# Kernel optimization log

Hardware: AMD Instinct MI355X
Metric: run time of the kernel (lower is better)

## Reference

```python
import jax, jax.numpy as jnp
import numpy as np

EMBED_DIM = 512
NUM_HEADS = 8
HEAD_DIM = EMBED_DIM // NUM_HEADS
SCALING = HEAD_DIM ** (-0.5)
LAMBDA = 1.0
T = 128
B = 8


def setup_inputs() -> dict:
    key = jax.random.key(0)
    ks = jax.random.split(key, 8)
    d = EMBED_DIM
    # xavier-uniform-ish scale for weights
    w_lim = float(np.sqrt(6.0 / (3 * d + d)))
    o_lim = float(np.sqrt(6.0 / (d + d)))
    return {
        "query": jax.random.normal(ks[0], (T, B, d), jnp.float32),
        "key": jax.random.normal(ks[1], (T, B, d), jnp.float32),
        "value": jax.random.normal(ks[2], (T, B, d), jnp.float32),
        "correlation_bias": jax.random.normal(ks[3], (B, T, T, T), jnp.float32) * 0.1,
        "in_proj_weight": jax.random.uniform(ks[4], (3 * d, d), jnp.float32, -w_lim, w_lim),
        "in_proj_bias": jnp.zeros((3 * d,), jnp.float32),
        "out_w": jax.random.uniform(ks[5], (d, d), jnp.float32, -o_lim, o_lim),
        "out_b": jnp.zeros((d,), jnp.float32),
    }


def reference(query, key, value, correlation_bias, in_proj_weight, in_proj_bias, out_w, out_b):
    tgt_len, bsz, d = query.shape
    h, hd = NUM_HEADS, HEAD_DIM
    # split packed in-projection
    q = query @ in_proj_weight[:d].T + in_proj_bias[:d]
    k = key @ in_proj_weight[d:2 * d].T + in_proj_bias[d:2 * d]
    v = value @ in_proj_weight[2 * d:].T + in_proj_bias[2 * d:]
    q = q * SCALING
    # [T, B, D] -> [B*H, T, hd]
    q = q.reshape(tgt_len, bsz * h, hd).transpose(1, 0, 2)
    k = k.reshape(tgt_len, bsz * h, hd).transpose(1, 0, 2)
    v = v.reshape(tgt_len, bsz * h, hd).transpose(1, 0, 2)
    # trilinear score cube: [B*H, Tq, Tk, Tv]
    scores = jnp.einsum('iat,ibt,ict->iabc', q, k, v)
    # expand correlation bias over heads: [B,Tq,Tk,Tv] -> [B*H,Tq,Tk,Tv]
    bias = jnp.broadcast_to(
        correlation_bias[:, None], (bsz, h, tgt_len, tgt_len, tgt_len)
    ).reshape(bsz * h, tgt_len, tgt_len, tgt_len)
    scores = scores + LAMBDA * bias
    # mean/max fusion over Tv, softmax over Tk
    fused = jnp.mean(scores, axis=-1) + jnp.max(scores, axis=-1)
    w = jax.nn.softmax(fused.astype(jnp.float32), axis=-1).astype(fused.dtype)
    # bmm with q (note: attends over q itself, Tk == Tq required)
    attn = jnp.einsum('iab,ibd->iad', w, q)
    attn = attn.transpose(1, 0, 2).reshape(tgt_len, bsz, d)
    return attn @ out_w.T + out_b
```

## Files before the change

### kernel.cpp

```cpp
#include <hip/hip_runtime.h>
#include <math.h>

#define SCALING 0.125f

typedef __attribute__((ext_vector_type(8))) short short8;
typedef __attribute__((ext_vector_type(4))) float f32x4;

static __device__ __forceinline__ unsigned short bf16r(float x) {
  unsigned int u = __float_as_uint(x);
  u += 0x7fffu + ((u >> 16) & 1u);
  return (unsigned short)(u >> 16);
}
static __device__ __forceinline__ float bf16f(unsigned short h) {
  return __uint_as_float(((unsigned int)h) << 16);
}
static __device__ __forceinline__ unsigned int pk_bf16(float lo, float hi) {
  unsigned int ua = __float_as_uint(lo);
  unsigned int ub = __float_as_uint(hi);
  ua += 0x7fffu + ((ua >> 16) & 1u);
  ub += 0x7fffu + ((ub >> 16) & 1u);
  return __builtin_amdgcn_perm(ub, ua, 0x07060302u);
}
static __device__ __forceinline__ void split4(float4 x, ushort4& h, ushort4& l) {
  h.x = bf16r(x.x); l.x = bf16r(x.x - bf16f(h.x));
  h.y = bf16r(x.y); l.y = bf16r(x.y - bf16f(h.y));
  h.z = bf16r(x.z); l.z = bf16r(x.z - bf16f(h.z));
  h.w = bf16r(x.w); l.w = bf16r(x.w - bf16f(h.w));
}
union U4S8 { uint4 u; short8 s; };

__global__ __launch_bounds__(256)
void prep_kernel(const float* __restrict__ query,
                 const float* __restrict__ key,
                 const float* __restrict__ value,
                 const float* __restrict__ W,
                 const float* __restrict__ out_w,
                 unsigned short* __restrict__ Xh,
                 unsigned short* __restrict__ Xl,
                 unsigned short* __restrict__ Wh,
                 unsigned short* __restrict__ Wl,
                 unsigned short* __restrict__ Owh,
                 unsigned short* __restrict__ Owl) {
  const int t = blockIdx.x * 256 + threadIdx.x;
  const int e = t * 4;
  const float* __restrict__ src;
  unsigned short *dh, *dl;
  if (e < 1572864) {
    const int g = e >> 19, j = e & 524287;
    src = (g == 0 ? query : g == 1 ? key : value) + j;
    dh = Xh + e; dl = Xl + e;
  } else if (e < 2359296) {
    const int j = e - 1572864;
    src = W + j; dh = Wh + j; dl = Wl + j;
  } else {
    const int j = e - 2359296;
    src = out_w + j; dh = Owh + j; dl = Owl + j;
  }
  const float4 v = *(const float4*)src;
  ushort4 hh, ll;
  split4(v, hh, ll);
  *(ushort4*)dh = hh;
  *(ushort4*)dl = ll;
}

__global__ __launch_bounds__(256)
void projmm_kernel(const unsigned short* __restrict__ Xh,
                   const unsigned short* __restrict__ Xl,
                   const unsigned short* __restrict__ Wh,
                   const unsigned short* __restrict__ Wl,
                   const float* __restrict__ bias,
                   float* __restrict__ qh, float* __restrict__ kh,
                   unsigned short* __restrict__ vh) {
  __shared__ __align__(16) unsigned short Ah[64 * 72];
  __shared__ __align__(16) unsigned short Al[64 * 72];
  __shared__ __align__(16) unsigned short Bh[64 * 72];
  __shared__ __align__(16) unsigned short Bl[64 * 72];
  const int n0 = blockIdx.x * 64;
  const int g = n0 >> 9;
  const unsigned short* __restrict__ Xgh = Xh + g * 524288;
  const unsigned short* __restrict__ Xgl = Xl + g * 524288;
  const int m0 = blockIdx.y * 64;
  const int tid = threadIdx.x;
  const int w = tid >> 6, lane = tid & 63;
  const int quad = lane >> 4, n15 = lane & 15;
  const int srow = tid >> 2;
  const int scol = (tid & 3) * 16;

  f32x4 acc[4];
#pragma unroll
  for (int nt = 0; nt < 4; ++nt) acc[nt] = (f32x4){0.f, 0.f, 0.f, 0.f};

  uint4 rah0, rah1, ral0, ral1, rbh0, rbh1, rbl0, rbl1;
  {
    const int ar = (m0 + srow) * 512 + scol;
    const int br = (n0 + srow) * 512 + scol;
    rah0 = *(const uint4*)&Xgh[ar];     rah1 = *(const uint4*)&Xgh[ar + 8];
    ral0 = *(const uint4*)&Xgl[ar];     ral1 = *(const uint4*)&Xgl[ar + 8];
    rbh0 = *(const uint4*)&Wh[br];      rbh1 = *(const uint4*)&Wh[br + 8];
    rbl0 = *(const uint4*)&Wl[br];      rbl1 = *(const uint4*)&Wl[br + 8];
  }

  for (int k0 = 0; k0 < 512; k0 += 64) {
    __syncthreads();
    *(uint4*)&Ah[srow * 72 + scol] = rah0; *(uint4*)&Ah[srow * 72 + scol + 8] = rah1;
    *(uint4*)&Al[srow * 72 + scol] = ral0; *(uint4*)&Al[srow * 72 + scol + 8] = ral1;
    *(uint4*)&Bh[srow * 72 + scol] = rbh0; *(uint4*)&Bh[srow * 72 + scol + 8] = rbh1;
    *(uint4*)&Bl[srow * 72 + scol] = rbl0; *(uint4*)&Bl[srow * 72 + scol + 8] = rbl1;
    __syncthreads();
    if (k0 + 64 < 512) {
      const int ar = (m0 + srow) * 512 + k0 + 64 + scol;
      const int br = (n0 + srow) * 512 + k0 + 64 + scol;
      rah0 = *(const uint4*)&Xgh[ar];   rah1 = *(const uint4*)&Xgh[ar + 8];
      ral0 = *(const uint4*)&Xgl[ar];   ral1 = *(const uint4*)&Xgl[ar + 8];
      rbh0 = *(const uint4*)&Wh[br];    rbh1 = *(const uint4*)&Wh[br + 8];
      rbl0 = *(const uint4*)&Wl[br];    rbl1 = *(const uint4*)&Wl[br + 8];
    }
#pragma unroll
    for (int kk = 0; kk < 2; ++kk) {
      short8 ah = *(const short8*)&Ah[(w * 16 + n15) * 72 + kk * 32 + quad * 8];
      short8 al = *(const short8*)&Al[(w * 16 + n15) * 72 + kk * 32 + quad * 8];
#pragma unroll
      for (int nt = 0; nt < 4; ++nt) {
        short8 bh = *(const short8*)&Bh[(nt * 16 + n15) * 72 + kk * 32 + quad * 8];
        short8 bl = *(const short8*)&Bl[(nt * 16 + n15) * 72 + kk * 32 + quad * 8];
        acc[nt] = __builtin_amdgcn_mfma_f32_16x16x32_bf16(ah, bh, acc[nt], 0, 0, 0);
        acc[nt] = __builtin_amdgcn_mfma_f32_16x16x32_bf16(ah, bl, acc[nt], 0, 0, 0);
        acc[nt] = __builtin_amdgcn_mfma_f32_16x16x32_bf16(al, bh, acc[nt], 0, 0, 0);
      }
    }
  }

#pragma unroll
  for (int nt = 0; nt < 4; ++nt) {
    const int j = n0 + nt * 16 + n15;
    const int jj = j & 511;
    const int head = jj >> 6;
    const int hd = jj & 63;
    const float bj = bias[j];
#pragma unroll
    for (int r = 0; r < 4; ++r) {
      const int row = m0 + w * 16 + quad * 4 + r;
      const int t = row >> 3;
      const int batch = row & 7;
      const int i = batch * 8 + head;
      const int idx = ((i << 7) + t) * 64 + hd;
      const float val = acc[nt][r] + bj;
      if (g == 0)      qh[idx] = val * SCALING;
      else if (g == 1) kh[idx] = val;
      else             vh[idx] = bf16r(val);
    }
  }
}

__global__ __launch_bounds__(256, 2)
void score_kernel(const float* __restrict__ qh,
                  const float* __restrict__ kh,
                  const unsigned short* __restrict__ vh,
                  const float* __restrict__ cbias,
                  unsigned short* __restrict__ attn_h,
                  unsigned short* __restrict__ attn_l) {
  __shared__ __align__(16) unsigned short Ks[2][128 * 72];
  __shared__ __align__(16) unsigned short Vs[2][128 * 72];
  __shared__ float rowS[8 * 128];

  const int ab = blockIdx.x;
  const int batch = ab >> 7;
  const int a = ab & 127;
  const int tid = threadIdx.x;
  const int w = tid >> 6;
  const int lane = tid & 63;
  const int quad = lane >> 4;
  const int n15 = lane & 15;
  const int col8 = (tid & 7) * 8;

  const float* __restrict__ bp = cbias + (size_t)ab * 16384;
  f32x4 biasReg[8][2];
#pragma unroll
  for (int ic = 0; ic < 8; ++ic)
#pragma unroll
    for (int jb = 0; jb < 2; ++jb) {
      const int b = w * 32 + jb * 16 + n15;
      biasReg[ic][jb] = *(const f32x4*)&bp[b * 128 + ic * 16 + quad * 4];
    }

  {
    const int i = batch * 8;
    const float* __restrict__ kb = kh + (size_t)i * 8192;
    const uint4* __restrict__ vb4 = (const uint4*)(vh + (size_t)i * 8192);
    const float* __restrict__ qa = qh + ((size_t)i * 128 + a) * 64;
    f32x4 q0 = *(const f32x4*)&qa[col8];
    f32x4 q1 = *(const f32x4*)&qa[col8 + 4];
#pragma unroll
    for (int j = 0; j < 4; ++j) {
      const int gg = j * 256 + tid;
      const int row = gg >> 3;
      *(uint4*)&Vs[0][row * 72 + col8] = vb4[gg];
      f32x4 k0 = *(const f32x4*)&kb[8 * gg];
      f32x4 k1 = *(const f32x4*)&kb[8 * gg + 4];
      k0 *= q0;
      k1 *= q1;
      uint4 pk;
      pk.x = pk_bf16(k0[0], k0[1]); pk.y = pk_bf16(k0[2], k0[3]);
      pk.z = pk_bf16(k1[0], k1[1]); pk.w = pk_bf16(k1[2], k1[3]);
      *(uint4*)&Ks[0][row * 72 + col8] = pk;
    }
  }
  __syncthreads();

  for (int h = 0; h < 8; ++h) {
    const int buf = h & 1;
    const int i = batch * 8 + h;

    uint4 vreg[4];
    f32x4 kreg[4][2];
    f32x4 qn0, qn1;
    if (h < 7) {
      const int in = i + 1;
      const float* __restrict__ kb = kh + (size_t)in * 8192;
      const uint4* __restrict__ vb4 = (const uint4*)(vh + (size_t)in * 8192);
      const float* __restrict__ qa = qh + ((size_t)in * 128 + a) * 64;
      qn0 = *(const f32x4*)&qa[col8];
      qn1 = *(const f32x4*)&qa[col8 + 4];
#pragma unroll
      for (int j = 0; j < 4; ++j) {
        const int gg = j * 256 + tid;
        vreg[j] = vb4[gg];
        kreg[j][0] = *(const f32x4*)&kb[8 * gg];
        kreg[j][1] = *(const f32x4*)&kb[8 * gg + 4];
      }
    }

    short8 bf[2][2];
#pragma unroll
    for (int jb = 0; jb < 2; ++jb)
#pragma unroll
      for (int kk = 0; kk < 2; ++kk)
        bf[jb][kk] = *(const short8*)&Ks[buf][(w * 32 + jb * 16 + n15) * 72 +
                                             kk * 32 + quad * 8];

    f32x4 acc[8][2];
#pragma unroll
    for (int ic = 0; ic < 8; ++ic)
#pragma unroll
      for (int jb = 0; jb < 2; ++jb) acc[ic][jb] = (f32x4){0.f, 0.f, 0.f, 0.f};
#pragma unroll
    for (int ic = 0; ic < 8; ++ic) {
      short8 a0 = *(const short8*)&Vs[buf][(ic * 16 + n15) * 72 + quad * 8];
      short8 a1 = *(const short8*)&Vs[buf][(ic * 16 + n15) * 72 + 32 + quad * 8];
      acc[ic][0] = __builtin_amdgcn_mfma_f32_16x16x32_bf16(a0, bf[0][0], acc[ic][0], 0, 0, 0);
      acc[ic][0] = __builtin_amdgcn_mfma_f32_16x16x32_bf16(a1, bf[0][1], acc[ic][0], 0, 0, 0);
      acc[ic][1] = __builtin_amdgcn_mfma_f32_16x16x32_bf16(a0, bf[1][0], acc[ic][1], 0, 0, 0);
      acc[ic][1] = __builtin_amdgcn_mfma_f32_16x16x32_bf16(a1, bf[1][1], acc[ic][1], 0, 0, 0);
    }

    if (h < 7) {
      const int nb = buf ^ 1;
#pragma unroll
      for (int j = 0; j < 4; ++j) {
        const int gg = j * 256 + tid;
        const int row = gg >> 3;
        *(uint4*)&Vs[nb][row * 72 + col8] = vreg[j];
        kreg[j][0] *= qn0;
        kreg[j][1] *= qn1;
        uint4 pk;
        pk.x = pk_bf16(kreg[j][0][0], kreg[j][0][1]);
        pk.y = pk_bf16(kreg[j][0][2], kreg[j][0][3]);
        pk.z = pk_bf16(kreg[j][1][0], kreg[j][1][1]);
        pk.w = pk_bf16(kreg[j][1][2], kreg[j][1][3]);
        *(uint4*)&Ks[nb][row * 72 + col8] = pk;
      }
    }

    float fsum[2] = {0.f, 0.f};
    float fmx[2] = {-INFINITY, -INFINITY};
#pragma unroll
    for (int ic = 0; ic < 8; ++ic)
#pragma unroll
      for (int jb = 0; jb < 2; ++jb) {
        const float v0 = acc[ic][jb][0] + biasReg[ic][jb][0];
        const float v1 = acc[ic][jb][1] + biasReg[ic][jb][1];
        const float v2 = acc[ic][jb][2] + biasReg[ic][jb][2];
        const float v3 = acc[ic][jb][3] + biasReg[ic][jb][3];
        fsum[jb] += (v0 + v1) + (v2 + v3);
        fmx[jb] = fmaxf(fmx[jb], fmaxf(fmaxf(v0, v1), fmaxf(v2, v3)));
      }
#pragma unroll
    for (int off = 16; off <= 32; off <<= 1) {
#pragma unroll
      for (int jb = 0; jb < 2; ++jb) {
        fsum[jb] += __shfl_xor(fsum[jb], off, 64);
        fmx[jb] = fmaxf(fmx[jb], __shfl_xor(fmx[jb], off, 64));
      }
    }
    if (quad == 0) {
      rowS[h * 128 + w * 32 + n15] = fsum[0] * (1.0f / 128.0f) + fmx[0];
      rowS[h * 128 + w * 32 + 16 + n15] = fsum[1] * (1.0f / 128.0f) + fmx[1];
    }

    __syncthreads();
  }

#pragma unroll
  for (int hh = 0; hh < 2; ++hh) {
    const int h = w * 2 + hh;
    const int i = batch * 8 + h;
    float f0 = rowS[h * 128 + lane], f1 = rowS[h * 128 + 64 + lane];
    float m = fmaxf(f0, f1);
#pragma unroll
    for (int off = 32; off >= 1; off >>= 1) m = fmaxf(m, __shfl_xor(m, off, 64));
    const float e0 = expf(f0 - m), e1 = expf(f1 - m);
    float s = e0 + e1;
#pragma unroll
    for (int off = 32; off >= 1; off >>= 1) s += __shfl_xor(s, off, 64);
    const float inv = 1.0f / s;
    rowS[h * 128 + lane] = e0 * inv;
    rowS[h * 128 + 64 + lane] = e1 * inv;
    const float* __restrict__ qp = qh + (size_t)i * 8192 + lane;
    float acc2 = 0.0f;
#pragma unroll 8
    for (int b = 0; b < 128; ++b)
      acc2 = fmaf(rowS[h * 128 + b], qp[b * 64], acc2);
    const size_t idx = ((size_t)a * 8 + batch) * 512 + h * 64 + lane;
    const unsigned short hi = bf16r(acc2);
    attn_h[idx] = hi;
    attn_l[idx] = bf16r(acc2 - bf16f(hi));
  }
}

__global__ __launch_bounds__(256)
void outmm_kernel(const unsigned short* __restrict__ Xah,
                  const unsigned short* __restrict__ Xal,
                  const unsigned short* __restrict__ Owh,
                  const unsigned short* __restrict__ Owl,
                  const float* __restrict__ bias,
                  float* __restrict__ out) {
  __shared__ __align__(16) unsigned short Ah[64 * 72];
  __shared__ __align__(16) unsigned short Al[64 * 72];
  __shared__ __align__(16) unsigned short Bh[32 * 72];
  __shared__ __align__(16) unsigned short Bl[32 * 72];
  const int n0 = blockIdx.x * 32;
  const int m0 = blockIdx.y * 64;
  const int tid = threadIdx.x;
  const int w = tid >> 6, lane = tid & 63;
  const int quad = lane >> 4, n15 = lane & 15;
  const int srow = tid >> 2;
  const int scol = (tid & 3) * 16;
  const bool doB = tid >= 128;
  const int brow = (tid & 127) >> 2;
  const int bcol = (tid & 3) * 16;

  f32x4 acc[2];
#pragma unroll
  for (int nt = 0; nt < 2; ++nt) acc[nt] = (f32x4){0.f, 0.f, 0.f, 0.f};

  uint4 rah0, rah1, ral0, ral1, rbh0, rbh1, rbl0, rbl1;
  {
    const int ar = (m0 + srow) * 512 + scol;
    rah0 = *(const uint4*)&Xah[ar];   rah1 = *(const uint4*)&Xah[ar + 8];
    ral0 = *(const uint4*)&Xal[ar];   ral1 = *(const uint4*)&Xal[ar + 8];
  }
  if (doB) {
    const int br = (n0 + brow) * 512 + bcol;
    rbh0 = *(const uint4*)&Owh[br];   rbh1 = *(const uint4*)&Owh[br + 8];
    rbl0 = *(const uint4*)&Owl[br];   rbl1 = *(const uint4*)&Owl[br + 8];
  }

  for (int k0 = 0; k0 < 512; k0 += 64) {
    __syncthreads();
    *(uint4*)&Ah[srow * 72 + scol] = rah0; *(uint4*)&Ah[srow * 72 + scol + 8] = rah1;
    *(uint4*)&Al[srow * 72 + scol] = ral0; *(uint4*)&Al[srow * 72 + scol + 8] = ral1;
    if (doB) {
      *(uint4*)&Bh[brow * 72 + bcol] = rbh0; *(uint4*)&Bh[brow * 72 + bcol + 8] = rbh1;
      *(uint4*)&Bl[brow * 72 + bcol] = rbl0; *(uint4*)&Bl[brow * 72 + bcol + 8] = rbl1;
    }
    __syncthreads();
    if (k0 + 64 < 512) {
      const int ar = (m0 + srow) * 512 + k0 + 64 + scol;
      rah0 = *(const uint4*)&Xah[ar]; rah1 = *(const uint4*)&Xah[ar + 8];
      ral0 = *(const uint4*)&Xal[ar]; ral1 = *(const uint4*)&Xal[ar + 8];
      if (doB) {
        const int br = (n0 + brow) * 512 + k0 + 64 + bcol;
        rbh0 = *(const uint4*)&Owh[br]; rbh1 = *(const uint4*)&Owh[br + 8];
        rbl0 = *(const uint4*)&Owl[br]; rbl1 = *(const uint4*)&Owl[br + 8];
      }
    }
#pragma unroll
    for (int kk = 0; kk < 2; ++kk) {
      short8 ah = *(const short8*)&Ah[(w * 16 + n15) * 72 + kk * 32 + quad * 8];
      short8 al = *(const short8*)&Al[(w * 16 + n15) * 72 + kk * 32 + quad * 8];
#pragma unroll
      for (int nt = 0; nt < 2; ++nt) {
        short8 bh = *(const short8*)&Bh[(nt * 16 + n15) * 72 + kk * 32 + quad * 8];
        short8 bl = *(const short8*)&Bl[(nt * 16 + n15) * 72 + kk * 32 + quad * 8];
        acc[nt] = __builtin_amdgcn_mfma_f32_16x16x32_bf16(ah, bh, acc[nt], 0, 0, 0);
        acc[nt] = __builtin_amdgcn_mfma_f32_16x16x32_bf16(ah, bl, acc[nt], 0, 0, 0);
        acc[nt] = __builtin_amdgcn_mfma_f32_16x16x32_bf16(al, bh, acc[nt], 0, 0, 0);
      }
    }
  }

#pragma unroll
  for (int nt = 0; nt < 2; ++nt) {
    const int j = n0 + nt * 16 + n15;
    const float bj = bias[j];
#pragma unroll
    for (int r = 0; r < 4; ++r) {
      const int row = m0 + w * 16 + quad * 4 + r;
      out[(size_t)row * 512 + j] = acc[nt][r] + bj;
    }
  }
}

extern "C" void kernel_launch(void* const* d_in, const int* in_sizes, int n_in,
                              void* d_out, int out_size, void* d_ws,
                              size_t ws_size, hipStream_t stream) {
  const float* query = (const float*)d_in[0];
  const float* key   = (const float*)d_in[1];
  const float* value = (const float*)d_in[2];
  const float* cbias = (const float*)d_in[3];
  const float* W     = (const float*)d_in[4];
  const float* pb    = (const float*)d_in[5];
  const float* out_w = (const float*)d_in[6];
  const float* out_b = (const float*)d_in[7];
  float* out = (float*)d_out;

  float* ws = (float*)d_ws;
  float* qh = ws;
  float* kh = ws + 524288;
  unsigned short* vh     = (unsigned short*)(ws + 1048576);
  unsigned short* attn_h = (unsigned short*)(ws + 1310720);
  unsigned short* attn_l = (unsigned short*)(ws + 1572864);
  unsigned short* Xh     = (unsigned short*)(ws + 1835008);
  unsigned short* Xl     = (unsigned short*)(ws + 2621440);
  unsigned short* Wh     = (unsigned short*)(ws + 3407872);
  unsigned short* Wl     = (unsigned short*)(ws + 3801088);
  unsigned short* Owh    = (unsigned short*)(ws + 4194304);
  unsigned short* Owl    = (unsigned short*)(ws + 4325376);

  prep_kernel<<<2560, 256, 0, stream>>>(query, key, value, W, out_w,
                                        Xh, Xl, Wh, Wl, Owh, Owl);
  projmm_kernel<<<dim3(24, 16), 256, 0, stream>>>(Xh, Xl, Wh, Wl, pb,
                                                  qh, kh, vh);
  score_kernel<<<1024, 256, 0, stream>>>(qh, kh, vh, cbias, attn_h, attn_l);
  outmm_kernel<<<dim3(16, 16), 256, 0, stream>>>(attn_h, attn_l, Owh, Owl,
                                                 out_b, out);
}
```

Baseline: 182.2 us.

## Load MFMA fragments directly from global memory, dropping LDS staging of K/V

The score kernel no longer stages q-scaled K and V tiles through double-buffered shared memory. Each wave now loads its own K rows and the V fragments straight from global memory into MFMA operand registers. The bias is folded in as the MFMA accumulator's initial value, and the per-head block barrier is replaced by a single barrier after the head loop. This removes LDS traffic, the barriers and most shared-memory usage, which may also allow more blocks per CU. In exchange, every wave re-reads the full V tile from cache, and the explicit software prefetch of the next head is lost.

After: 230.1 us. 1.26x slower.

```diff
diff --git a/kernel.cpp b/kernel.cpp
--- a/kernel.cpp
+++ b/kernel.cpp
@@ -159,8 +159,6 @@
                   const float* __restrict__ cbias,
                   unsigned short* __restrict__ attn_h,
                   unsigned short* __restrict__ attn_l) {
-  __shared__ __align__(16) unsigned short Ks[2][128 * 72];
-  __shared__ __align__(16) unsigned short Vs[2][128 * 72];
   __shared__ float rowS[8 * 128];
 
   const int ab = blockIdx.x;
@@ -171,7 +169,6 @@
   const int lane = tid & 63;
   const int quad = lane >> 4;
   const int n15 = lane & 15;
-  const int col8 = (tid & 7) * 8;
 
   const float* __restrict__ bp = cbias + (size_t)ab * 16384;
   f32x4 biasReg[8][2];
@@ -183,107 +180,52 @@
       biasReg[ic][jb] = *(const f32x4*)&bp[b * 128 + ic * 16 + quad * 4];
     }
 
-  {
-    const int i = batch * 8;
+  for (int h = 0; h < 8; ++h) {
+    const int i = batch * 8 + h;
     const float* __restrict__ kb = kh + (size_t)i * 8192;
-    const uint4* __restrict__ vb4 = (const uint4*)(vh + (size_t)i * 8192);
     const float* __restrict__ qa = qh + ((size_t)i * 128 + a) * 64;
-    f32x4 q0 = *(const f32x4*)&qa[col8];
-    f32x4 q1 = *(const f32x4*)&qa[col8 + 4];
-#pragma unroll
-    for (int j = 0; j < 4; ++j) {
-      const int gg = j * 256 + tid;
-      const int row = gg >> 3;
-      *(uint4*)&Vs[0][row * 72 + col8] = vb4[gg];
-      f32x4 k0 = *(const f32x4*)&kb[8 * gg];
-      f32x4 k1 = *(const f32x4*)&kb[8 * gg + 4];
-      k0 *= q0;
-      k1 *= q1;
-      uint4 pk;
-      pk.x = pk_bf16(k0[0], k0[1]); pk.y = pk_bf16(k0[2], k0[3]);
-      pk.z = pk_bf16(k1[0], k1[1]); pk.w = pk_bf16(k1[2], k1[3]);
-      *(uint4*)&Ks[0][row * 72 + col8] = pk;
-    }
-  }
-  __syncthreads();
-
-  for (int h = 0; h < 8; ++h) {
-    const int buf = h & 1;
-    const int i = batch * 8 + h;
-
-    uint4 vreg[4];
-    f32x4 kreg[4][2];
-    f32x4 qn0, qn1;
-    if (h < 7) {
-      const int in = i + 1;
-      const float* __restrict__ kb = kh + (size_t)in * 8192;
-      const uint4* __restrict__ vb4 = (const uint4*)(vh + (size_t)in * 8192);
-      const float* __restrict__ qa = qh + ((size_t)in * 128 + a) * 64;
-      qn0 = *(const f32x4*)&qa[col8];
-      qn1 = *(const f32x4*)&qa[col8 + 4];
-#pragma unroll
-      for (int j = 0; j < 4; ++j) {
-        const int gg = j * 256 + tid;
-        vreg[j] = vb4[gg];
-        kreg[j][0] = *(const f32x4*)&kb[8 * gg];
-        kreg[j][1] = *(const f32x4*)&kb[8 * gg + 4];
-      }
-    }
+    const unsigned short* __restrict__ vb = vh + (size_t)i * 8192;
+
+    f32x4 q00 = *(const f32x4*)&qa[quad * 8];
+    f32x4 q01 = *(const f32x4*)&qa[quad * 8 + 4];
+    f32x4 q10 = *(const f32x4*)&qa[32 + quad * 8];
+    f32x4 q11 = *(const f32x4*)&qa[32 + quad * 8 + 4];
 
     short8 bf[2][2];
 #pragma unroll
-    for (int jb = 0; jb < 2; ++jb)
-#pragma unroll
-      for (int kk = 0; kk < 2; ++kk)
-        bf[jb][kk] = *(const short8*)&Ks[buf][(w * 32 + jb * 16 + n15) * 72 +
-                                             kk * 32 + quad * 8];
-
-    f32x4 acc[8][2];
-#pragma unroll
-    for (int ic = 0; ic < 8; ++ic)
-#pragma unroll
-      for (int jb = 0; jb < 2; ++jb) acc[ic][jb] = (f32x4){0.f, 0.f, 0.f, 0.f};
-#pragma unroll
-    for (int ic = 0; ic < 8; ++ic) {
-      short8 a0 = *(const short8*)&Vs[buf][(ic * 16 + n15) * 72 + quad * 8];
-      short8 a1 = *(const short8*)&Vs[buf][(ic * 16 + n15) * 72 + 32 + quad * 8];
-      acc[ic][0] = __builtin_amdgcn_mfma_f32_16x16x32_bf16(a0, bf[0][0], acc[ic][0], 0, 0, 0);
-      acc[ic][0] = __builtin_amdgcn_mfma_f32_16x16x32_bf16(a1, bf[0][1], acc[ic][0], 0, 0, 0);
-      acc[ic][1] = __builtin_amdgcn_mfma_f32_16x16x32_bf16(a0, bf[1][0], acc[ic][1], 0, 0, 0);
-      acc[ic][1] = __builtin_amdgcn_mfma_f32_16x16x32_bf16(a1, bf[1][1], acc[ic][1], 0, 0, 0);
-    }
-
-    if (h < 7) {
-      const int nb = buf ^ 1;
-#pragma unroll
-      for (int j = 0; j < 4; ++j) {
-        const int gg = j * 256 + tid;
-        const int row = gg >> 3;
-        *(uint4*)&Vs[nb][row * 72 + col8] = vreg[j];
-        kreg[j][0] *= qn0;
-        kreg[j][1] *= qn1;
-        uint4 pk;
-        pk.x = pk_bf16(kreg[j][0][0], kreg[j][0][1]);
-        pk.y = pk_bf16(kreg[j][0][2], kreg[j][0][3]);
-        pk.z = pk_bf16(kreg[j][1][0], kreg[j][1][1]);
-        pk.w = pk_bf16(kreg[j][1][2], kreg[j][1][3]);
-        *(uint4*)&Ks[nb][row * 72 + col8] = pk;
-      }
+    for (int jb = 0; jb < 2; ++jb) {
+      const int b = w * 32 + jb * 16 + n15;
+      f32x4 k00 = *(const f32x4*)&kb[b * 64 + quad * 8];
+      f32x4 k01 = *(const f32x4*)&kb[b * 64 + quad * 8 + 4];
+      f32x4 k10 = *(const f32x4*)&kb[b * 64 + 32 + quad * 8];
+      f32x4 k11 = *(const f32x4*)&kb[b * 64 + 32 + quad * 8 + 4];
+      k00 *= q00; k01 *= q01; k10 *= q10; k11 *= q11;
+      U4S8 u0, u1;
+      u0.u.x = pk_bf16(k00[0], k00[1]); u0.u.y = pk_bf16(k00[2], k00[3]);
+      u0.u.z = pk_bf16(k01[0], k01[1]); u0.u.w = pk_bf16(k01[2], k01[3]);
+      u1.u.x = pk_bf16(k10[0], k10[1]); u1.u.y = pk_bf16(k10[2], k10[3]);
+      u1.u.z = pk_bf16(k11[0], k11[1]); u1.u.w = pk_bf16(k11[2], k11[3]);
+      bf[jb][0] = u0.s;
+      bf[jb][1] = u1.s;
     }
 
     float fsum[2] = {0.f, 0.f};
     float fmx[2] = {-INFINITY, -INFINITY};
 #pragma unroll
-    for (int ic = 0; ic < 8; ++ic)
+    for (int ic = 0; ic < 8; ++ic) {
+      short8 a0 = *(const short8*)&vb[(ic * 16 + n15) * 64 + quad * 8];
+      short8 a1 = *(const short8*)&vb[(ic * 16 + n15) * 64 + 32 + quad * 8];
 #pragma unroll
       for (int jb = 0; jb < 2; ++jb) {
-        const float v0 = acc[ic][jb][0] + biasReg[ic][jb][0];
-        const float v1 = acc[ic][jb][1] + biasReg[ic][jb][1];
-        const float v2 = acc[ic][jb][2] + biasReg[ic][jb][2];
-        const float v3 = acc[ic][jb][3] + biasReg[ic][jb][3];
+        f32x4 t = __builtin_amdgcn_mfma_f32_16x16x32_bf16(a0, bf[jb][0],
+                                                          biasReg[ic][jb], 0, 0, 0);
+        f32x4 acc = __builtin_amdgcn_mfma_f32_16x16x32_bf16(a1, bf[jb][1], t, 0, 0, 0);
+        const float v0 = acc[0], v1 = acc[1], v2 = acc[2], v3 = acc[3];
         fsum[jb] += (v0 + v1) + (v2 + v3);
-        fmx[jb] = fmaxf(fmx[jb], fmaxf(fmaxf(v0, v1), fmaxf(v2, v3)));
-      }
+        const float m01 = fmaxf(v0, v1), m23 = fmaxf(v2, v3);
+        fmx[jb] = fmaxf(fmaxf(m01, m23), fmx[jb]);
+      }
+    }
 #pragma unroll
     for (int off = 16; off <= 32; off <<= 1) {
 #pragma unroll
@@ -296,9 +238,8 @@
       rowS[h * 128 + w * 32 + n15] = fsum[0] * (1.0f / 128.0f) + fmx[0];
       rowS[h * 128 + w * 32 + 16 + n15] = fsum[1] * (1.0f / 128.0f) + fmx[1];
     }
-
-    __syncthreads();
-  }
+  }
+  __syncthreads();
 
 #pragma unroll
   for (int hh = 0; hh < 2; ++hh) {
```

## Replace LDS-tiled projection GEMMs with direct-from-global 16x16 MFMA tiles

Applied to the files above, without the earlier changes.

Both the input projection and output projection GEMMs drop shared-memory staging and barriers. Each wave now loads its MFMA operands straight from global memory and computes a single 16x16 output tile, with smaller per-block tiles and grids grown to match. This removes LDS traffic and __syncthreads overhead and raises block count for occupancy. In exchange it gives up operand reuse across waves and leans on L2/L1 caching, since each A/B row is re-read by many waves.

New measurement: 220.2 us. +20.9%, slower.

```diff
diff --git a/kernel.cpp b/kernel.cpp
--- a/kernel.cpp
+++ b/kernel.cpp
@@ -71,84 +71,49 @@
                    const float* __restrict__ bias,
                    float* __restrict__ qh, float* __restrict__ kh,
                    unsigned short* __restrict__ vh) {
-  __shared__ __align__(16) unsigned short Ah[64 * 72];
-  __shared__ __align__(16) unsigned short Al[64 * 72];
-  __shared__ __align__(16) unsigned short Bh[64 * 72];
-  __shared__ __align__(16) unsigned short Bl[64 * 72];
-  const int n0 = blockIdx.x * 64;
+  const int n0 = blockIdx.x * 16;
   const int g = n0 >> 9;
-  const unsigned short* __restrict__ Xgh = Xh + g * 524288;
-  const unsigned short* __restrict__ Xgl = Xl + g * 524288;
-  const int m0 = blockIdx.y * 64;
   const int tid = threadIdx.x;
   const int w = tid >> 6, lane = tid & 63;
   const int quad = lane >> 4, n15 = lane & 15;
-  const int srow = tid >> 2;
-  const int scol = (tid & 3) * 16;
-
-  f32x4 acc[4];
-#pragma unroll
-  for (int nt = 0; nt < 4; ++nt) acc[nt] = (f32x4){0.f, 0.f, 0.f, 0.f};
-
-  uint4 rah0, rah1, ral0, ral1, rbh0, rbh1, rbl0, rbl1;
-  {
-    const int ar = (m0 + srow) * 512 + scol;
-    const int br = (n0 + srow) * 512 + scol;
-    rah0 = *(const uint4*)&Xgh[ar];     rah1 = *(const uint4*)&Xgh[ar + 8];
-    ral0 = *(const uint4*)&Xgl[ar];     ral1 = *(const uint4*)&Xgl[ar + 8];
-    rbh0 = *(const uint4*)&Wh[br];      rbh1 = *(const uint4*)&Wh[br + 8];
-    rbl0 = *(const uint4*)&Wl[br];      rbl1 = *(const uint4*)&Wl[br + 8];
-  }
-
-  for (int k0 = 0; k0 < 512; k0 += 64) {
-    __syncthreads();
-    *(uint4*)&Ah[srow * 72 + scol] = rah0; *(uint4*)&Ah[srow * 72 + scol + 8] = rah1;
-    *(uint4*)&Al[srow * 72 + scol] = ral0; *(uint4*)&Al[srow * 72 + scol + 8] = ral1;
-    *(uint4*)&Bh[srow * 72 + scol] = rbh0; *(uint4*)&Bh[srow * 72 + scol + 8] = rbh1;
-    *(uint4*)&Bl[srow * 72 + scol] = rbl0; *(uint4*)&Bl[srow * 72 + scol + 8] = rbl1;
-    __syncthreads();
-    if (k0 + 64 < 512) {
-      const int ar = (m0 + srow) * 512 + k0 + 64 + scol;
-      const int br = (n0 + srow) * 512 + k0 + 64 + scol;
-      rah0 = *(const uint4*)&Xgh[ar];   rah1 = *(const uint4*)&Xgh[ar + 8];
-      ral0 = *(const uint4*)&Xgl[ar];   ral1 = *(const uint4*)&Xgl[ar + 8];
-      rbh0 = *(const uint4*)&Wh[br];    rbh1 = *(const uint4*)&Wh[br + 8];
-      rbl0 = *(const uint4*)&Wl[br];    rbl1 = *(const uint4*)&Wl[br + 8];
-    }
-#pragma unroll
-    for (int kk = 0; kk < 2; ++kk) {
-      short8 ah = *(const short8*)&Ah[(w * 16 + n15) * 72 + kk * 32 + quad * 8];
-      short8 al = *(const short8*)&Al[(w * 16 + n15) * 72 + kk * 32 + quad * 8];
-#pragma unroll
-      for (int nt = 0; nt < 4; ++nt) {
-        short8 bh = *(const short8*)&Bh[(nt * 16 + n15) * 72 + kk * 32 + quad * 8];
-        short8 bl = *(const short8*)&Bl[(nt * 16 + n15) * 72 + kk * 32 + quad * 8];
-        acc[nt] = __builtin_amdgcn_mfma_f32_16x16x32_bf16(ah, bh, acc[nt], 0, 0, 0);
-        acc[nt] = __builtin_amdgcn_mfma_f32_16x16x32_bf16(ah, bl, acc[nt], 0, 0, 0);
-        acc[nt] = __builtin_amdgcn_mfma_f32_16x16x32_bf16(al, bh, acc[nt], 0, 0, 0);
-      }
-    }
-  }
-
-#pragma unroll
-  for (int nt = 0; nt < 4; ++nt) {
-    const int j = n0 + nt * 16 + n15;
-    const int jj = j & 511;
-    const int head = jj >> 6;
-    const int hd = jj & 63;
-    const float bj = bias[j];
-#pragma unroll
-    for (int r = 0; r < 4; ++r) {
-      const int row = m0 + w * 16 + quad * 4 + r;
-      const int t = row >> 3;
-      const int batch = row & 7;
-      const int i = batch * 8 + head;
-      const int idx = ((i << 7) + t) * 64 + hd;
-      const float val = acc[nt][r] + bj;
-      if (g == 0)      qh[idx] = val * SCALING;
-      else if (g == 1) kh[idx] = val;
-      else             vh[idx] = bf16r(val);
-    }
+  const int m0 = blockIdx.y * 64 + w * 16;
+
+  const unsigned short* __restrict__ Ah_ = Xh + (size_t)g * 524288 +
+                                           (size_t)(m0 + n15) * 512;
+  const unsigned short* __restrict__ Al_ = Xl + (size_t)g * 524288 +
+                                           (size_t)(m0 + n15) * 512;
+  const unsigned short* __restrict__ Bh_ = Wh + (size_t)(n0 + n15) * 512;
+  const unsigned short* __restrict__ Bl_ = Wl + (size_t)(n0 + n15) * 512;
+  const int q8 = quad * 8;
+
+  f32x4 acc = (f32x4){0.f, 0.f, 0.f, 0.f};
+#pragma unroll 4
+  for (int k0 = 0; k0 < 512; k0 += 32) {
+    short8 ah = *(const short8*)&Ah_[k0 + q8];
+    short8 al = *(const short8*)&Al_[k0 + q8];
+    short8 bh = *(const short8*)&Bh_[k0 + q8];
+    short8 bl = *(const short8*)&Bl_[k0 + q8];
+    acc = __builtin_amdgcn_mfma_f32_16x16x32_bf16(ah, bh, acc, 0, 0, 0);
+    acc = __builtin_amdgcn_mfma_f32_16x16x32_bf16(ah, bl, acc, 0, 0, 0);
+    acc = __builtin_amdgcn_mfma_f32_16x16x32_bf16(al, bh, acc, 0, 0, 0);
+  }
+
+  const int j = n0 + n15;
+  const int jj = j & 511;
+  const int head = jj >> 6;
+  const int hd = jj & 63;
+  const float bj = bias[j];
+#pragma unroll
+  for (int r = 0; r < 4; ++r) {
+    const int row = m0 + quad * 4 + r;
+    const int t = row >> 3;
+    const int batch = row & 7;
+    const int i = batch * 8 + head;
+    const int idx = ((i << 7) + t) * 64 + hd;
+    const float val = acc[r] + bj;
+    if (g == 0)      qh[idx] = val * SCALING;
+    else if (g == 1) kh[idx] = val;
+    else             vh[idx] = bf16r(val);
   }
 }
 
@@ -334,80 +299,36 @@
                   const unsigned short* __restrict__ Owl,
                   const float* __restrict__ bias,
                   float* __restrict__ out) {
-  __shared__ __align__(16) unsigned short Ah[64 * 72];
-  __shared__ __align__(16) unsigned short Al[64 * 72];
-  __shared__ __align__(16) unsigned short Bh[32 * 72];
-  __shared__ __align__(16) unsigned short Bl[32 * 72];
-  const int n0 = blockIdx.x * 32;
-  const int m0 = blockIdx.y * 64;
+  const int n0 = blockIdx.x * 16;
   const int tid = threadIdx.x;
   const int w = tid >> 6, lane = tid & 63;
   const int quad = lane >> 4, n15 = lane & 15;
-  const int srow = tid >> 2;
-  const int scol = (tid & 3) * 16;
-  const bool doB = tid >= 128;
-  const int brow = (tid & 127) >> 2;
-  const int bcol = (tid & 3) * 16;
-
-  f32x4 acc[2];
-#pragma unroll
-  for (int nt = 0; nt < 2; ++nt) acc[nt] = (f32x4){0.f, 0.f, 0.f, 0.f};
-
-  uint4 rah0, rah1, ral0, ral1, rbh0, rbh1, rbl0, rbl1;
-  {
-    const int ar = (m0 + srow) * 512 + scol;
-    rah0 = *(const uint4*)&Xah[ar];   rah1 = *(const uint4*)&Xah[ar + 8];
-    ral0 = *(const uint4*)&Xal[ar];   ral1 = *(const uint4*)&Xal[ar + 8];
-  }
-  if (doB) {
-    const int br = (n0 + brow) * 512 + bcol;
-    rbh0 = *(const uint4*)&Owh[br];   rbh1 = *(const uint4*)&Owh[br + 8];
-    rbl0 = *(const uint4*)&Owl[br];   rbl1 = *(const uint4*)&Owl[br + 8];
-  }
-
-  for (int k0 = 0; k0 < 512; k0 += 64) {
-    __syncthreads();
-    *(uint4*)&Ah[srow * 72 + scol] = rah0; *(uint4*)&Ah[srow * 72 + scol + 8] = rah1;
-    *(uint4*)&Al[srow * 72 + scol] = ral0; *(uint4*)&Al[srow * 72 + scol + 8] = ral1;
-    if (doB) {
-      *(uint4*)&Bh[brow * 72 + bcol] = rbh0; *(uint4*)&Bh[brow * 72 + bcol + 8] = rbh1;
-      *(uint4*)&Bl[brow * 72 + bcol] = rbl0; *(uint4*)&Bl[brow * 72 + bcol + 8] = rbl1;
-    }
-    __syncthreads();
-    if (k0 + 64 < 512) {
-      const int ar = (m0 + srow) * 512 + k0 + 64 + scol;
-      rah0 = *(const uint4*)&Xah[ar]; rah1 = *(const uint4*)&Xah[ar + 8];
-      ral0 = *(const uint4*)&Xal[ar]; ral1 = *(const uint4*)&Xal[ar + 8];
-      if (doB) {
-        const int br = (n0 + brow) * 512 + k0 + 64 + bcol;
-        rbh0 = *(const uint4*)&Owh[br]; rbh1 = *(const uint4*)&Owh[br + 8];
-        rbl0 = *(const uint4*)&Owl[br]; rbl1 = *(const uint4*)&Owl[br + 8];
-      }
-    }
-#pragma unroll
-    for (int kk = 0; kk < 2; ++kk) {
-      short8 ah = *(const short8*)&Ah[(w * 16 + n15) * 72 + kk * 32 + quad * 8];
-      short8 al = *(const short8*)&Al[(w * 16 + n15) * 72 + kk * 32 + quad * 8];
-#pragma unroll
-      for (int nt = 0; nt < 2; ++nt) {
-        short8 bh = *(const short8*)&Bh[(nt * 16 + n15) * 72 + kk * 32 + quad * 8];
-        short8 bl = *(const short8*)&Bl[(nt * 16 + n15) * 72 + kk * 32 + quad * 8];
-        acc[nt] = __builtin_amdgcn_mfma_f32_16x16x32_bf16(ah, bh, acc[nt], 0, 0, 0);
-        acc[nt] = __builtin_amdgcn_mfma_f32_16x16x32_bf16(ah, bl, acc[nt], 0, 0, 0);
-        acc[nt] = __builtin_amdgcn_mfma_f32_16x16x32_bf16(al, bh, acc[nt], 0, 0, 0);
-      }
-    }
-  }
-
-#pragma unroll
-  for (int nt = 0; nt < 2; ++nt) {
-    const int j = n0 + nt * 16 + n15;
-    const float bj = bias[j];
-#pragma unroll
-    for (int r = 0; r < 4; ++r) {
-      const int row = m0 + w * 16 + quad * 4 + r;
-      out[(size_t)row * 512 + j] = acc[nt][r] + bj;
-    }
+  const int m0 = blockIdx.y * 64 + w * 16;
+
+  const unsigned short* __restrict__ Ah_ = Xah + (size_t)(m0 + n15) * 512;
+  const unsigned short* __restrict__ Al_ = Xal + (size_t)(m0 + n15) * 512;
+  const unsigned short* __restrict__ Bh_ = Owh + (size_t)(n0 + n15) * 512;
+  const unsigned short* __restrict__ Bl_ = Owl + (size_t)(n0 + n15) * 512;
+  const int q8 = quad * 8;
+
+  f32x4 acc = (f32x4){0.f, 0.f, 0.f, 0.f};
+#pragma unroll 4
+  for (int k0 = 0; k0 < 512; k0 += 32) {
+    short8 ah = *(const short8*)&Ah_[k0 + q8];
+    short8 al = *(const short8*)&Al_[k0 + q8];
+    short8 bh = *(const short8*)&Bh_[k0 + q8];
+    short8 bl = *(const short8*)&Bl_[k0 + q8];
+    acc = __builtin_amdgcn_mfma_f32_16x16x32_bf16(ah, bh, acc, 0, 0, 0);
+    acc = __builtin_amdgcn_mfma_f32_16x16x32_bf16(ah, bl, acc, 0, 0, 0);
+    acc = __builtin_amdgcn_mfma_f32_16x16x32_bf16(al, bh, acc, 0, 0, 0);
+  }
+
+  const int j = n0 + n15;
+  const float bj = bias[j];
+#pragma unroll
+  for (int r = 0; r < 4; ++r) {
+    const int row = m0 + quad * 4 + r;
+    out[(size_t)row * 512 + j] = acc[r] + bj;
   }
 }
 
@@ -439,9 +360,9 @@
 
   prep_kernel<<<2560, 256, 0, stream>>>(query, key, value, W, out_w,
                                         Xh, Xl, Wh, Wl, Owh, Owl);
-  projmm_kernel<<<dim3(24, 16), 256, 0, stream>>>(Xh, Xl, Wh, Wl, pb,
+  projmm_kernel<<<dim3(96, 16), 256, 0, stream>>>(Xh, Xl, Wh, Wl, pb,
                                                   qh, kh, vh);
   score_kernel<<<1024, 256, 0, stream>>>(qh, kh, vh, cbias, attn_h, attn_l);
-  outmm_kernel<<<dim3(16, 16), 256, 0, stream>>>(attn_h, attn_l, Owh, Owl,
+  outmm_kernel<<<dim3(32, 16), 256, 0, stream>>>(attn_h, attn_l, Owh, Owl,
                                                  out_b, out);
 }
```
